# Kernel optimization log

Measured on AMD Instinct MI355X. Metric: run time of the kernel, lower is better.

The kernel has to match this reference:

```python
import jax, jax.numpy as jnp
import numpy as np

N_Q, M, D, DV = 4096, 32768, 512, 512  # groups, keys, key dim, value dim


def setup_inputs() -> dict:
    key = jax.random.key(0)
    k1, k2, k3 = jax.random.split(key, 3)
    query = jax.random.normal(k1, (N_Q, D), dtype=jnp.float32)
    keys = jax.random.normal(k2, (M, D), dtype=jnp.float32)
    values = jax.random.normal(k3, (M, DV), dtype=jnp.float32)
    # each query/group owns exactly M//N_Q keys -> no empty softmax rows
    tree_idx = jnp.arange(M, dtype=jnp.int32) % N_Q
    return {"query": query, "keys": keys, "values": values, "tree_idx": tree_idx}


def _l2_normalize(x, eps=1e-12):
    # matches F.normalize(x, dim=1, p=2): x / max(||x||_2, eps)
    n = jnp.linalg.norm(x, axis=1, keepdims=True)
    return x / jnp.maximum(n, eps)


def reference(query, keys, values, tree_idx):
    n_q = query.shape[0]
    # mask[q, m] = (tree_idx[m] == q); equivalent to zeros.index_add(0, tree_idx, eye(M)).bool()
    mask = tree_idx[None, :] == jnp.arange(n_q, dtype=tree_idx.dtype)[:, None]  # [N_q, M]
    query_n = _l2_normalize(query)
    keys_n = _l2_normalize(keys)
    align = query_n @ keys_n.T                      # [N_q, M] cosine similarities
    align = jnp.where(mask, align, -jnp.inf)        # masked_fill_(~mask, -inf)
    alpha = jax.nn.softmax(align, axis=1)           # segment-masked softmax per query
    att = alpha @ values                            # [N_q, DV]
    return att, alpha.sum(axis=0)
```

## Files before the change

### kernel.cpp

```cpp
#include <hip/hip_runtime.h>
#include <math.h>

#define D_DIM 512
#define BK_T 1024
#define LDS_CNT_CAP 14336

__device__ __forceinline__ float d4(const float4& a, const float4& b) {
    return a.x*b.x + a.y*b.y + a.z*b.z + a.w*b.w;
}
__device__ __forceinline__ void fma4(float4& a, float w, const float4& v) {
    a.x += w*v.x; a.y += w*v.y; a.z += w*v.z; a.w += w*v.w;
}

__global__ __launch_bounds__(BK_T) void build_keylist(
        const int* __restrict__ tree_idx, int m_total, int n_q,
        int* __restrict__ offsets, int* __restrict__ keylist,
        int* __restrict__ gcnt ) {
    extern __shared__ int lds[];
    int* wsum = lds;
    int* cnt  = (n_q <= LDS_CNT_CAP) ? (lds + 16) : gcnt;
    const int tid  = threadIdx.x;
    const int lane = tid & 63;
    const int wv   = tid >> 6;

    for (int i = tid; i < n_q; i += BK_T) cnt[i] = 0;
    __syncthreads();

    const int m4 = m_total >> 2;
    const int4* t4 = (const int4*)tree_idx;
    for (int i = tid; i < m4; i += BK_T) {
        int4 v = t4[i];
        atomicAdd(&cnt[v.x], 1); atomicAdd(&cnt[v.y], 1);
        atomicAdd(&cnt[v.z], 1); atomicAdd(&cnt[v.w], 1);
    }
    for (int i = (m4 << 2) + tid; i < m_total; i += BK_T)
        atomicAdd(&cnt[tree_idx[i]], 1);
    __syncthreads();

    const int items = (n_q + BK_T - 1) / BK_T;
    const int base  = tid * items;
    int local = 0;
    for (int i = 0; i < items; ++i) {
        int idx = base + i;
        if (idx < n_q) local += cnt[idx];
    }
    int incl = local;
#pragma unroll
    for (int o = 1; o < 64; o <<= 1) {
        int v = __shfl_up(incl, o);
        if (lane >= o) incl += v;
    }
    if (lane == 63) wsum[wv] = incl;
    __syncthreads();
    if (wv == 0) {
        int v = (lane < 16) ? wsum[lane] : 0;
        int iv = v;
#pragma unroll
        for (int o = 1; o < 16; o <<= 1) {
            int t = __shfl_up(iv, o);
            if (lane >= o) iv += t;
        }
        if (lane < 16) wsum[lane] = iv - v;
    }
    __syncthreads();
    int run = wsum[wv] + incl - local;
    for (int i = 0; i < items; ++i) {
        int idx = base + i;
        if (idx < n_q) {
            int c = cnt[idx];
            offsets[idx] = run;
            cnt[idx] = run;
            run += c;
        }
    }
    if (tid == BK_T - 1) offsets[n_q] = run;
    __syncthreads();

    for (int i = tid; i < m_total; i += BK_T) {
        int t = tree_idx[i];
        int p = atomicAdd(&cnt[t], 1);
        keylist[p] = i;
    }
}

__global__ __launch_bounds__(256, 8) void attn_main(
        const float* __restrict__ query, const float* __restrict__ keys,
        const float* __restrict__ values, const int* __restrict__ offsets,
        const int* __restrict__ keylist, float* __restrict__ att,
        float* __restrict__ colsum, int n_q) {
    __shared__ float4 s_acc[2][128];
    __shared__ float  s_ps[2][2];
    const int lane = threadIdx.x & 63;
    const int wv   = threadIdx.x >> 6;
    const int ql   = wv >> 1;
    const int h    = wv & 1;
    const int qi   = (blockIdx.x << 1) + ql;
    const bool act = qi < n_q;

    float e0 = 0.f, e1 = 0.f, e2 = 0.f, e3 = 0.f;
    int   m0 = 0, m1 = 0, m2 = 0, m3 = 0;
    float4 aa = make_float4(0.f, 0.f, 0.f, 0.f);
    float4 ab = make_float4(0.f, 0.f, 0.f, 0.f);
    int off = 0, nk = 0;
    bool fast = false;

    if (act) {
        off  = offsets[qi];
        nk   = offsets[qi + 1] - off;
        fast = (nk == 8);
        const float4* qp = (const float4*)(query + (size_t)qi * D_DIM);
        float4 qa = qp[lane], qb = qp[lane + 64];
        float pq = d4(qa, qa) + d4(qb, qb);
        float psum = 0.f;

        if (fast) {
            m0 = keylist[off + h];     m1 = keylist[off + h + 2];
            m2 = keylist[off + h + 4]; m3 = keylist[off + h + 6];
            const float4* k0 = (const float4*)(keys + (size_t)m0 * D_DIM);
            const float4* k1 = (const float4*)(keys + (size_t)m1 * D_DIM);
            const float4* k2 = (const float4*)(keys + (size_t)m2 * D_DIM);
            const float4* k3 = (const float4*)(keys + (size_t)m3 * D_DIM);
            float4 x0a = k0[lane], x0b = k0[lane + 64];
            float4 x1a = k1[lane], x1b = k1[lane + 64];
            float pd0 = d4(qa, x0a) + d4(qb, x0b), pk0 = d4(x0a, x0a) + d4(x0b, x0b);
            float pd1 = d4(qa, x1a) + d4(qb, x1b), pk1 = d4(x1a, x1a) + d4(x1b, x1b);
            float4 x2a = k2[lane], x2b = k2[lane + 64];
            float4 x3a = k3[lane], x3b = k3[lane + 64];
            float pd2 = d4(qa, x2a) + d4(qb, x2b), pk2 = d4(x2a, x2a) + d4(x2b, x2b);
            float pd3 = d4(qa, x3a) + d4(qb, x3b), pk3 = d4(x3a, x3a) + d4(x3b, x3b);
#pragma unroll
            for (int o = 32; o > 0; o >>= 1) {
                pq  += __shfl_xor(pq,  o);
                pd0 += __shfl_xor(pd0, o); pk0 += __shfl_xor(pk0, o);
                pd1 += __shfl_xor(pd1, o); pk1 += __shfl_xor(pk1, o);
                pd2 += __shfl_xor(pd2, o); pk2 += __shfl_xor(pk2, o);
                pd3 += __shfl_xor(pd3, o); pk3 += __shfl_xor(pk3, o);
            }
            const float qinv = 1.0f / fmaxf(sqrtf(pq), 1e-12f);
            e0 = __expf(pd0 * qinv / fmaxf(sqrtf(pk0), 1e-12f));
            e1 = __expf(pd1 * qinv / fmaxf(sqrtf(pk1), 1e-12f));
            e2 = __expf(pd2 * qinv / fmaxf(sqrtf(pk2), 1e-12f));
            e3 = __expf(pd3 * qinv / fmaxf(sqrtf(pk3), 1e-12f));
            psum = e0 + e1 + e2 + e3;
            if (lane == 0) s_ps[ql][h] = psum;
            const float4* v0 = (const float4*)(values + (size_t)m0 * D_DIM);
            const float4* v1 = (const float4*)(values + (size_t)m1 * D_DIM);
            const float4* v2 = (const float4*)(values + (size_t)m2 * D_DIM);
            const float4* v3 = (const float4*)(values + (size_t)m3 * D_DIM);
            float4 y0a = v0[lane], y0b = v0[lane + 64];
            float4 y1a = v1[lane], y1b = v1[lane + 64];
            fma4(aa, e0, y0a); fma4(ab, e0, y0b);
            fma4(aa, e1, y1a); fma4(ab, e1, y1b);
            float4 y2a = v2[lane], y2b = v2[lane + 64];
            float4 y3a = v3[lane], y3b = v3[lane + 64];
            fma4(aa, e2, y2a); fma4(ab, e2, y2b);
            fma4(aa, e3, y3a); fma4(ab, e3, y3b);
        } else {
#pragma unroll
            for (int o = 32; o > 0; o >>= 1) pq += __shfl_xor(pq, o);
            const float qinv = 1.0f / fmaxf(sqrtf(pq), 1e-12f);
            for (int j = h; j < nk; j += 2) {
                int mi = keylist[off + j];
                const float4* kp = (const float4*)(keys   + (size_t)mi * D_DIM);
                const float4* vp = (const float4*)(values + (size_t)mi * D_DIM);
                float4 ka = kp[lane], kb = kp[lane + 64];
                float pd = d4(qa, ka) + d4(qb, kb);
                float pk = d4(ka, ka) + d4(kb, kb);
#pragma unroll
                for (int o = 32; o > 0; o >>= 1) {
                    pd += __shfl_xor(pd, o);
                    pk += __shfl_xor(pk, o);
                }
                float e = __expf(pd * qinv / fmaxf(sqrtf(pk), 1e-12f));
                psum += e;
                if (lane == 0) colsum[mi] = e;
                float4 va = vp[lane], vb = vp[lane + 64];
                fma4(aa, e, va); fma4(ab, e, vb);
            }
            if (lane == 0) s_ps[ql][h] = psum;
        }
        if (h == 0) { s_acc[ql][lane] = aa; s_acc[ql][64 + lane] = ab; }
    }
    __syncthreads();
    if (act) {
        const float tot = s_ps[ql][0] + s_ps[ql][1];
        const float inv = (tot > 0.f) ? 1.0f / tot : 0.f;
        if (h == 1) {
            float4 oa = s_acc[ql][lane], ob = s_acc[ql][64 + lane];
            oa.x = (oa.x + aa.x) * inv; oa.y = (oa.y + aa.y) * inv;
            oa.z = (oa.z + aa.z) * inv; oa.w = (oa.w + aa.w) * inv;
            ob.x = (ob.x + ab.x) * inv; ob.y = (ob.y + ab.y) * inv;
            ob.z = (ob.z + ab.z) * inv; ob.w = (ob.w + ab.w) * inv;
            float4* op = (float4*)(att + (size_t)qi * D_DIM);
            op[lane]      = oa;
            op[lane + 64] = ob;
        }
        if (fast) {
            if (lane == 0) {
                colsum[m0] = e0 * inv; colsum[m1] = e1 * inv;
                colsum[m2] = e2 * inv; colsum[m3] = e3 * inv;
            }
        } else if (lane == 0) {
            for (int j = h; j < nk; j += 2) colsum[keylist[off + j]] *= inv;
        }
    }
}

extern "C" void kernel_launch(void* const* d_in, const int* in_sizes, int n_in,
                              void* d_out, int out_size, void* d_ws, size_t ws_size,
                              hipStream_t stream) {
    const float* query    = (const float*)d_in[0];
    const float* keys     = (const float*)d_in[1];
    const float* values   = (const float*)d_in[2];
    const int*   tree_idx = (const int*)d_in[3];

    const int n_q     = in_sizes[0] / D_DIM;
    const int m_total = in_sizes[3];

    float* att    = (float*)d_out;
    float* colsum = att + (size_t)n_q * D_DIM;

    int* offsets = (int*)d_ws;
    int* keylist = offsets + n_q + 1;
    int* gcnt    = keylist + m_total;

    const size_t lds_bytes =
        (size_t)(16 + ((n_q <= LDS_CNT_CAP) ? n_q : 0)) * sizeof(int);
    build_keylist<<<1, BK_T, lds_bytes, stream>>>(tree_idx, m_total, n_q,
                                                  offsets, keylist, gcnt);
    attn_main<<<(n_q + 1) / 2, 256, 0, stream>>>(query, keys, values, offsets,
                                                 keylist, att, colsum, n_q);
}
```

Baseline: 194.1 us.

## Split keylist build into multi-block kernels and use one block per query

The single-block keylist builder becomes four grid-wide kernels (zero, count, scan, scatter), so counting and scattering run across many blocks instead of one 1024-thread block. The attention kernel now gives each query its own 512-thread block, with 8 waves each taking one key and reducing partial sums through LDS. The specialized 8-key fast path is removed. The costs are extra kernel launches, global atomics in place of LDS atomics, and larger blocks that might lower occupancy.

```diff
diff --git a/kernel.cpp b/kernel.cpp
--- a/kernel.cpp
+++ b/kernel.cpp
@@ -2,43 +2,32 @@
 #include <math.h>
 
 #define D_DIM 512
-#define BK_T 1024
-#define LDS_CNT_CAP 14336
 
 __device__ __forceinline__ float d4(const float4& a, const float4& b) {
     return a.x*b.x + a.y*b.y + a.z*b.z + a.w*b.w;
 }
-__device__ __forceinline__ void fma4(float4& a, float w, const float4& v) {
-    a.x += w*v.x; a.y += w*v.y; a.z += w*v.z; a.w += w*v.w;
+
+__global__ void k_zero(int* cnt, int n) {
+    int i = blockIdx.x * blockDim.x + threadIdx.x;
+    if (i < n) cnt[i] = 0;
 }
-
-__global__ __launch_bounds__(BK_T) void build_keylist(
-        const int* __restrict__ tree_idx, int m_total, int n_q,
-        int* __restrict__ offsets, int* __restrict__ keylist,
-        int* __restrict__ gcnt ) {
-    extern __shared__ int lds[];
-    int* wsum = lds;
-    int* cnt  = (n_q <= LDS_CNT_CAP) ? (lds + 16) : gcnt;
-    const int tid  = threadIdx.x;
-    const int lane = tid & 63;
-    const int wv   = tid >> 6;
-
-    for (int i = tid; i < n_q; i += BK_T) cnt[i] = 0;
-    __syncthreads();
-
-    const int m4 = m_total >> 2;
-    const int4* t4 = (const int4*)tree_idx;
-    for (int i = tid; i < m4; i += BK_T) {
-        int4 v = t4[i];
+__global__ void k_count(const int* __restrict__ t, int* __restrict__ cnt, int m) {
+    int i = blockIdx.x * blockDim.x + threadIdx.x;
+    int i4 = i << 2;
+    if (i4 + 3 < m) {
+        int4 v = ((const int4*)t)[i];
         atomicAdd(&cnt[v.x], 1); atomicAdd(&cnt[v.y], 1);
         atomicAdd(&cnt[v.z], 1); atomicAdd(&cnt[v.w], 1);
+    } else {
+        for (int k = i4; k < m; ++k) atomicAdd(&cnt[t[k]], 1);
     }
-    for (int i = (m4 << 2) + tid; i < m_total; i += BK_T)
-        atomicAdd(&cnt[tree_idx[i]], 1);
-    __syncthreads();
-
-    const int items = (n_q + BK_T - 1) / BK_T;
-    const int base  = tid * items;
+}
+__global__ __launch_bounds__(1024) void k_scan(int* __restrict__ cnt,
+                                               int* __restrict__ offsets, int n_q) {
+    __shared__ int wsum[16];
+    const int tid = threadIdx.x, lane = tid & 63, wv = tid >> 6;
+    const int items = (n_q + 1023) >> 10;
+    const int base = tid * items;
     int local = 0;
     for (int i = 0; i < items; ++i) {
         int idx = base + i;
@@ -73,136 +62,85 @@
             run += c;
         }
     }
-    if (tid == BK_T - 1) offsets[n_q] = run;
-    __syncthreads();
-
-    for (int i = tid; i < m_total; i += BK_T) {
-        int t = tree_idx[i];
-        int p = atomicAdd(&cnt[t], 1);
+    if (tid == 1023) offsets[n_q] = run;
+}
+__global__ void k_scatter(const int* __restrict__ t, int* __restrict__ cnt,
+                          int* __restrict__ keylist, int m) {
+    int i = blockIdx.x * blockDim.x + threadIdx.x;
+    if (i < m) {
+        int p = atomicAdd(&cnt[t[i]], 1);
         keylist[p] = i;
     }
 }
 
-__global__ __launch_bounds__(256, 8) void attn_main(
+__global__ __launch_bounds__(512, 8) void attn_block(
         const float* __restrict__ query, const float* __restrict__ keys,
         const float* __restrict__ values, const int* __restrict__ offsets,
         const int* __restrict__ keylist, float* __restrict__ att,
-        float* __restrict__ colsum, int n_q) {
-    __shared__ float4 s_acc[2][128];
-    __shared__ float  s_ps[2][2];
-    const int lane = threadIdx.x & 63;
-    const int wv   = threadIdx.x >> 6;
-    const int ql   = wv >> 1;
-    const int h    = wv & 1;
-    const int qi   = (blockIdx.x << 1) + ql;
-    const bool act = qi < n_q;
+        float* __restrict__ colsum) {
+    __shared__ float4 s_v[8][128];
+    __shared__ float  s_e[8];
 
-    float e0 = 0.f, e1 = 0.f, e2 = 0.f, e3 = 0.f;
-    int   m0 = 0, m1 = 0, m2 = 0, m3 = 0;
+    const int qi   = blockIdx.x;
+    const int tid  = threadIdx.x;
+    const int lane = tid & 63;
+    const int wv   = tid >> 6;
+
+    const int off = offsets[qi];
+    const int nk  = offsets[qi + 1] - off;
+
+    const float4* qp = (const float4*)(query + (size_t)qi * D_DIM);
+    float4 qa = qp[lane], qb = qp[lane + 64];
+    float pq = d4(qa, qa) + d4(qb, qb);
+
     float4 aa = make_float4(0.f, 0.f, 0.f, 0.f);
     float4 ab = make_float4(0.f, 0.f, 0.f, 0.f);
-    int off = 0, nk = 0;
-    bool fast = false;
+    float esum = 0.f;
 
-    if (act) {
-        off  = offsets[qi];
-        nk   = offsets[qi + 1] - off;
-        fast = (nk == 8);
-        const float4* qp = (const float4*)(query + (size_t)qi * D_DIM);
-        float4 qa = qp[lane], qb = qp[lane + 64];
-        float pq = d4(qa, qa) + d4(qb, qb);
-        float psum = 0.f;
+    for (int idx = wv; idx < nk; idx += 8) {
+        const int mi = keylist[off + idx];
+        const float4* kp = (const float4*)(keys   + (size_t)mi * D_DIM);
+        const float4* vp = (const float4*)(values + (size_t)mi * D_DIM);
+        float4 ka = kp[lane], kb = kp[lane + 64];
+        float4 va = vp[lane], vb = vp[lane + 64];
+        float pd = d4(qa, ka) + d4(qb, kb);
+        float pk = d4(ka, ka) + d4(kb, kb);
+        float pq2 = pq;
+#pragma unroll
+        for (int o = 32; o > 0; o >>= 1) {
+            pd  += __shfl_xor(pd,  o);
+            pk  += __shfl_xor(pk,  o);
+            pq2 += __shfl_xor(pq2, o);
+        }
+        const float qinv = 1.0f / fmaxf(sqrtf(pq2), 1e-12f);
+        const float e = __expf(pd * qinv / fmaxf(sqrtf(pk), 1e-12f));
+        esum += e;
+        if (lane == 0) colsum[mi] = e;
+        aa.x += e*va.x; aa.y += e*va.y; aa.z += e*va.z; aa.w += e*va.w;
+        ab.x += e*vb.x; ab.y += e*vb.y; ab.z += e*vb.z; ab.w += e*vb.w;
+    }
 
-        if (fast) {
-            m0 = keylist[off + h];     m1 = keylist[off + h + 2];
-            m2 = keylist[off + h + 4]; m3 = keylist[off + h + 6];
-            const float4* k0 = (const float4*)(keys + (size_t)m0 * D_DIM);
-            const float4* k1 = (const float4*)(keys + (size_t)m1 * D_DIM);
-            const float4* k2 = (const float4*)(keys + (size_t)m2 * D_DIM);
-            const float4* k3 = (const float4*)(keys + (size_t)m3 * D_DIM);
-            float4 x0a = k0[lane], x0b = k0[lane + 64];
-            float4 x1a = k1[lane], x1b = k1[lane + 64];
-            float pd0 = d4(qa, x0a) + d4(qb, x0b), pk0 = d4(x0a, x0a) + d4(x0b, x0b);
-            float pd1 = d4(qa, x1a) + d4(qb, x1b), pk1 = d4(x1a, x1a) + d4(x1b, x1b);
-            float4 x2a = k2[lane], x2b = k2[lane + 64];
-            float4 x3a = k3[lane], x3b = k3[lane + 64];
-            float pd2 = d4(qa, x2a) + d4(qb, x2b), pk2 = d4(x2a, x2a) + d4(x2b, x2b);
-            float pd3 = d4(qa, x3a) + d4(qb, x3b), pk3 = d4(x3a, x3a) + d4(x3b, x3b);
+    if (lane == 0) s_e[wv] = esum;
+    s_v[wv][lane]      = aa;
+    s_v[wv][64 + lane] = ab;
+    __syncthreads();
+
+    const float tot = s_e[0] + s_e[1] + s_e[2] + s_e[3]
+                    + s_e[4] + s_e[5] + s_e[6] + s_e[7];
+    const float inv = (tot > 0.f) ? 1.0f / tot : 0.f;
+
+    if (tid < 128) {
+        float4 r = s_v[0][tid];
 #pragma unroll
-            for (int o = 32; o > 0; o >>= 1) {
-                pq  += __shfl_xor(pq,  o);
-                pd0 += __shfl_xor(pd0, o); pk0 += __shfl_xor(pk0, o);
-                pd1 += __shfl_xor(pd1, o); pk1 += __shfl_xor(pk1, o);
-                pd2 += __shfl_xor(pd2, o); pk2 += __shfl_xor(pk2, o);
-                pd3 += __shfl_xor(pd3, o); pk3 += __shfl_xor(pk3, o);
-            }
-            const float qinv = 1.0f / fmaxf(sqrtf(pq), 1e-12f);
-            e0 = __expf(pd0 * qinv / fmaxf(sqrtf(pk0), 1e-12f));
-            e1 = __expf(pd1 * qinv / fmaxf(sqrtf(pk1), 1e-12f));
-            e2 = __expf(pd2 * qinv / fmaxf(sqrtf(pk2), 1e-12f));
-            e3 = __expf(pd3 * qinv / fmaxf(sqrtf(pk3), 1e-12f));
-            psum = e0 + e1 + e2 + e3;
-            if (lane == 0) s_ps[ql][h] = psum;
-            const float4* v0 = (const float4*)(values + (size_t)m0 * D_DIM);
-            const float4* v1 = (const float4*)(values + (size_t)m1 * D_DIM);
-            const float4* v2 = (const float4*)(values + (size_t)m2 * D_DIM);
-            const float4* v3 = (const float4*)(values + (size_t)m3 * D_DIM);
-            float4 y0a = v0[lane], y0b = v0[lane + 64];
-            float4 y1a = v1[lane], y1b = v1[lane + 64];
-            fma4(aa, e0, y0a); fma4(ab, e0, y0b);
-            fma4(aa, e1, y1a); fma4(ab, e1, y1b);
-            float4 y2a = v2[lane], y2b = v2[lane + 64];
-            float4 y3a = v3[lane], y3b = v3[lane + 64];
-            fma4(aa, e2, y2a); fma4(ab, e2, y2b);
-            fma4(aa, e3, y3a); fma4(ab, e3, y3b);
-        } else {
-#pragma unroll
-            for (int o = 32; o > 0; o >>= 1) pq += __shfl_xor(pq, o);
-            const float qinv = 1.0f / fmaxf(sqrtf(pq), 1e-12f);
-            for (int j = h; j < nk; j += 2) {
-                int mi = keylist[off + j];
-                const float4* kp = (const float4*)(keys   + (size_t)mi * D_DIM);
-                const float4* vp = (const float4*)(values + (size_t)mi * D_DIM);
-                float4 ka = kp[lane], kb = kp[lane + 64];
-                float pd = d4(qa, ka) + d4(qb, kb);
-                float pk = d4(ka, ka) + d4(kb, kb);
-#pragma unroll
-                for (int o = 32; o > 0; o >>= 1) {
-                    pd += __shfl_xor(pd, o);
-                    pk += __shfl_xor(pk, o);
-                }
-                float e = __expf(pd * qinv / fmaxf(sqrtf(pk), 1e-12f));
-                psum += e;
-                if (lane == 0) colsum[mi] = e;
-                float4 va = vp[lane], vb = vp[lane + 64];
-                fma4(aa, e, va); fma4(ab, e, vb);
-            }
-            if (lane == 0) s_ps[ql][h] = psum;
+        for (int j = 1; j < 8; ++j) {
+            float4 p = s_v[j][tid];
+            r.x += p.x; r.y += p.y; r.z += p.z; r.w += p.w;
         }
-        if (h == 0) { s_acc[ql][lane] = aa; s_acc[ql][64 + lane] = ab; }
+        r.x *= inv; r.y *= inv; r.z *= inv; r.w *= inv;
+        ((float4*)(att + (size_t)qi * D_DIM))[tid] = r;
     }
-    __syncthreads();
-    if (act) {
-        const float tot = s_ps[ql][0] + s_ps[ql][1];
-        const float inv = (tot > 0.f) ? 1.0f / tot : 0.f;
-        if (h == 1) {
-            float4 oa = s_acc[ql][lane], ob = s_acc[ql][64 + lane];
-            oa.x = (oa.x + aa.x) * inv; oa.y = (oa.y + aa.y) * inv;
-            oa.z = (oa.z + aa.z) * inv; oa.w = (oa.w + aa.w) * inv;
-            ob.x = (ob.x + ab.x) * inv; ob.y = (ob.y + ab.y) * inv;
-            ob.z = (ob.z + ab.z) * inv; ob.w = (ob.w + ab.w) * inv;
-            float4* op = (float4*)(att + (size_t)qi * D_DIM);
-            op[lane]      = oa;
-            op[lane + 64] = ob;
-        }
-        if (fast) {
-            if (lane == 0) {
-                colsum[m0] = e0 * inv; colsum[m1] = e1 * inv;
-                colsum[m2] = e2 * inv; colsum[m3] = e3 * inv;
-            }
-        } else if (lane == 0) {
-            for (int j = h; j < nk; j += 2) colsum[keylist[off + j]] *= inv;
-        }
+    if (lane == 0) {
+        for (int idx = wv; idx < nk; idx += 8) colsum[keylist[off + idx]] *= inv;
     }
 }
 
@@ -220,14 +158,14 @@
     float* att    = (float*)d_out;
     float* colsum = att + (size_t)n_q * D_DIM;
 
-    int* offsets = (int*)d_ws;
+    int* cnt     = (int*)d_ws;
+    int* offsets = cnt + n_q;
     int* keylist = offsets + n_q + 1;
-    int* gcnt    = keylist + m_total;
 
-    const size_t lds_bytes =
-        (size_t)(16 + ((n_q <= LDS_CNT_CAP) ? n_q : 0)) * sizeof(int);
-    build_keylist<<<1, BK_T, lds_bytes, stream>>>(tree_idx, m_total, n_q,
-                                                  offsets, keylist, gcnt);
-    attn_main<<<(n_q + 1) / 2, 256, 0, stream>>>(query, keys, values, offsets,
-                                                 keylist, att, colsum, n_q);
+    k_zero   <<<(n_q + 255) / 256, 256, 0, stream>>>(cnt, n_q);
+    k_count  <<<((m_total >> 2) + 255) / 256, 256, 0, stream>>>(tree_idx, cnt, m_total);
+    k_scan   <<<1, 1024, 0, stream>>>(cnt, offsets, n_q);
+    k_scatter<<<(m_total + 255) / 256, 256, 0, stream>>>(tree_idx, cnt, keylist, m_total);
+    attn_block<<<n_q, 512, 0, stream>>>(query, keys, values, offsets, keylist,
+                                        att, colsum);
 }
```

Measured after the change: 177.2 us. -8.7%, faster.
